# Kernel optimization log

Measured on AMD Instinct MI355X. Metric: run time of the kernel, lower is better.

## Reference

```python
import jax, jax.numpy as jnp
import numpy as np

NUM_TAGS = 32            # init arg
N = NUM_TAGS + 2         # internal num_tags (start/end appended)
START = N - 2
END = N - 1
B = 1024
T = 1024
NEG = -6969.0            # module's 'minus infinity' constant


def setup_inputs() -> dict:
    key = jax.random.key(0)
    k1, k2 = jax.random.split(key)
    features = jax.random.normal(k1, (B, T, N), dtype=jnp.float32)
    # learned parameter: transition matrix [N, N]
    transitions = jax.random.normal(k2, (N, N), dtype=jnp.float32)
    return {"features": features, "transitions": transitions}


def _viterbi(features, transitions):
    # features: [B, T, N]; transitions: [N, N]
    Bn, Tn, Nn = features.shape
    init = jnp.full((Bn, Nn), NEG, dtype=features.dtype).at[:, START].set(0.0)

    def step(scores, feat):
        # score[b, j, k] = scores[b, k] + feat[b, j] + transitions[j, k]
        sc = scores[:, None, :] + feat[:, :, None] + transitions[None, :, :]
        return jnp.max(sc, axis=-1), jnp.argmax(sc, axis=-1)

    feats_t = jnp.swapaxes(features, 0, 1)            # [T, B, N]
    scores, paths = jax.lax.scan(step, init, feats_t)  # paths: [T, B, N] int

    scores = scores + transitions[END]                # add transition to end tag
    best = jnp.max(scores, axis=-1)                   # [B]
    idx = jnp.argmax(scores, axis=-1)                 # [B]

    # backtrack through backpointers, from t = T-1 down to 0
    def back(i, path):
        ni = jnp.take_along_axis(path, i[:, None], axis=1)[:, 0]
        return ni, ni

    _, tags = jax.lax.scan(back, idx, paths, reverse=True)  # tags: [T, B]
    best_path = jnp.concatenate([tags.T, idx[:, None]], axis=1)  # [B, T+1]
    return best, best_path


def reference(features, transitions):
    return _viterbi(features, transitions)
```

## Files before the change

### kernel.cpp

```cpp
#include <hip/hip_runtime.h>
#include <stdint.h>

#define BB 1024
#define TT 1024
#define NN 34
#define NEGV -6969.0f

typedef float v2f __attribute__((ext_vector_type(2)));
typedef float v4f __attribute__((ext_vector_type(4)));

__device__ __forceinline__ float fmax3(float a, float b, float c) {
    return fmaxf(fmaxf(a, b), c);
}

__global__ __launch_bounds__(256, 1) void viterbi_wave(
        const float* __restrict__ feat,
        const float* __restrict__ trans,
        unsigned char* __restrict__ bpg,
        float* __restrict__ out)
{
    __shared__ __align__(16) float sc[4][64];
    __shared__ unsigned char Fm[4][16][NN];
    __shared__ int Eb[4][16];

    const int wid  = threadIdx.x >> 6;
    const int lane = threadIdx.x & 63;
    const int j    = lane;
    const int jm   = (j < NN) ? j : (NN - 1);
    const bool act = (j < NN);
    const int bg   = blockIdx.x * 4 + wid;

    v4f t4[8]; v2f t2;
    {
        const float* trow = trans + jm * NN;
#pragma unroll
        for (int i = 0; i < 8; ++i)
            t4[i] = (v4f){trow[4*i], trow[4*i+1], trow[4*i+2], trow[4*i+3]};
        t2 = (v2f){trow[32], trow[33]};
    }
    v4f e4[8]; v2f e2;
    {
        const float* erow = trans + (NN - 1) * NN;
#pragma unroll
        for (int i = 0; i < 8; ++i)
            e4[i] = (v4f){erow[4*i], erow[4*i+1], erow[4*i+2], erow[4*i+3]};
        e2 = (v2f){erow[32], erow[33]};
    }

    const float* fp = feat + (size_t)bg * TT * NN + jm;
    unsigned char* bpt = bpg + (size_t)bg * TT * NN + j;

    float* const scW = &sc[wid][0];
    const v4f* const S4 = (const v4f*)scW;
    const v2f* const S2 = (const v2f*)scW;

    scW[lane] = (lane == 32) ? 0.0f : NEGV;

    v4f q[8]; v2f q8;
#pragma unroll
    for (int i = 0; i < 8; ++i) q[i] = S4[i];
    q8 = S2[16];

    float fr0 = fp[0*NN], fr1 = fp[1*NN], fr2 = fp[2*NN], fr3 = fp[3*NN];

    auto vstep = [&](float fv, unsigned char* bpw) {
        const v4f f4 = (v4f){fv, fv, fv, fv};
        const v2f f2 = (v2f){fv, fv};
        v4f w[8]; v2f w8;
#pragma unroll
        for (int i = 0; i < 8; ++i) w[i] = (q[i] + f4) + t4[i];
        w8 = (q8 + f2) + t2;
        float wv[NN];
#pragma unroll
        for (int i = 0; i < 8; ++i) {
            wv[4*i+0] = w[i].x; wv[4*i+1] = w[i].y;
            wv[4*i+2] = w[i].z; wv[4*i+3] = w[i].w;
        }
        wv[32] = w8.x; wv[33] = w8.y;
        float a[12];
#pragma unroll
        for (int i = 0; i < 11; ++i) a[i] = fmax3(wv[3*i], wv[3*i+1], wv[3*i+2]);
        a[11] = wv[33];
        float b0 = fmax3(a[0], a[1], a[2]), b1 = fmax3(a[3], a[4], a[5]);
        float b2 = fmax3(a[6], a[7], a[8]), b3 = fmax3(a[9], a[10], a[11]);
        float m = fmaxf(fmaxf(b0, b1), fmaxf(b2, b3));
        scW[lane] = m;
#pragma unroll
        for (int i = 0; i < 8; ++i) q[i] = S4[i];
        q8 = S2[16];
        int am = 127;
#pragma unroll
        for (int k = NN - 1; k >= 0; --k) am = (wv[k] == m) ? k : am;
        if (act) *bpw = (unsigned char)am;
    };

    for (int n = 0; n < 255; ++n) {
        { float f = fr0; fr0 = fp[4*NN]; vstep(f, bpt + 0*NN); }
        { float f = fr1; fr1 = fp[5*NN]; vstep(f, bpt + 1*NN); }
        { float f = fr2; fr2 = fp[6*NN]; vstep(f, bpt + 2*NN); }
        { float f = fr3; fr3 = fp[7*NN]; vstep(f, bpt + 3*NN); }
        fp += 4*NN; bpt += 4*NN;
    }
    vstep(fr0, bpt + 0*NN);
    vstep(fr1, bpt + 1*NN);
    vstep(fr2, bpt + 2*NN);
    vstep(fr3, bpt + 3*NN);

    int bi;
    float bm;
    {
        v4f w[8]; v2f w8;
#pragma unroll
        for (int i = 0; i < 8; ++i) w[i] = q[i] + e4[i];
        w8 = q8 + e2;
        float wv[NN];
#pragma unroll
        for (int i = 0; i < 8; ++i) {
            wv[4*i+0] = w[i].x; wv[4*i+1] = w[i].y;
            wv[4*i+2] = w[i].z; wv[4*i+3] = w[i].w;
        }
        wv[32] = w8.x; wv[33] = w8.y;
        float a[12];
#pragma unroll
        for (int i = 0; i < 11; ++i) a[i] = fmax3(wv[3*i], wv[3*i+1], wv[3*i+2]);
        a[11] = wv[33];
        float b0 = fmax3(a[0], a[1], a[2]), b1 = fmax3(a[3], a[4], a[5]);
        float b2 = fmax3(a[6], a[7], a[8]), b3 = fmax3(a[9], a[10], a[11]);
        bm = fmaxf(fmaxf(b0, b1), fmaxf(b2, b3));
        bi = 127;
#pragma unroll
        for (int k = NN - 1; k >= 0; --k) bi = (wv[k] == bm) ? k : bi;
    }
    if (lane == 0) out[bg] = bm;

    asm volatile("s_waitcnt vmcnt(0)" ::: "memory");
    const unsigned char* __restrict__ bb = bpg + (size_t)bg * TT * NN;

    {
        const int c = lane >> 2;
        const int sub = lane & 3;
        int mv[9];
#pragma unroll
        for (int qi = 0; qi < 9; ++qi) {
            int x = sub + 4 * qi;
            mv[qi] = (x < NN) ? x : (NN - 1);
        }
        const unsigned char* cb = bb + (size_t)c * 64 * NN;
        for (int i = 63; i >= 0; --i) {
            const unsigned char* rb = cb + (size_t)i * NN;
#pragma unroll
            for (int qi = 0; qi < 9; ++qi) mv[qi] = rb[mv[qi]];
        }
#pragma unroll
        for (int qi = 0; qi < 9; ++qi) {
            int x = sub + 4 * qi;
            if (x < NN) Fm[wid][c][x] = (unsigned char)mv[qi];
        }
    }

    if (lane == 0) {
        int e = bi;
        Eb[wid][15] = e;
        for (int c = 15; c >= 1; --c) { e = Fm[wid][c][e]; Eb[wid][c - 1] = e; }
    }

    float* po = out + BB + (size_t)bg * (TT + 1);
    if (lane < 16) {
        int c = lane;
        int m = Eb[wid][c];
        for (int i = 63; i >= 0; --i) {
            m = bb[(size_t)((c * 64 + i) * NN) + m];
            po[c * 64 + i] = (float)m;
        }
    }
    if (lane == 16) po[TT] = (float)bi;
}

extern "C" void kernel_launch(void* const* d_in, const int* in_sizes, int n_in,
                              void* d_out, int out_size, void* d_ws, size_t ws_size,
                              hipStream_t stream) {
    const float* feat  = (const float*)d_in[0];
    const float* trans = (const float*)d_in[1];
    float* out = (float*)d_out;
    unsigned char* bp = (unsigned char*)d_ws;

    viterbi_wave<<<BB / 4, 256, 0, stream>>>(feat, trans, bp, out);
}
```

Baseline: 626.8 us.

## Launch one wave per block and tree-reduce the argmax

Changes the launch from 256-thread blocks holding four independent waves to 64-thread blocks with one wave each, so there are 1024 blocks instead of 256 and waves are scheduled independently. The serial 34-step argmax select chain is replaced by a compare-to-index pass followed by a min3 tree reduction, which shortens the dependency chain on the per-step critical path. A scheduling barrier is added after the shared-memory reload, and the end-transition row is read from global memory at the end rather than held in registers, which lowers register pressure during the main loop. The trade-off is more instructions per step for the argmax and a shift in how waves are placed across CUs.

```diff
diff --git a/kernel.cpp b/kernel.cpp
--- a/kernel.cpp
+++ b/kernel.cpp
@@ -12,23 +12,26 @@
 __device__ __forceinline__ float fmax3(float a, float b, float c) {
     return fmaxf(fmaxf(a, b), c);
 }
+__device__ __forceinline__ int imin2(int a, int b) { return a < b ? a : b; }
+__device__ __forceinline__ int imin3(int a, int b, int c) {
+    return imin2(imin2(a, b), c);
+}
 
-__global__ __launch_bounds__(256, 1) void viterbi_wave(
+__global__ __launch_bounds__(64, 1) void viterbi_wave(
         const float* __restrict__ feat,
         const float* __restrict__ trans,
         unsigned char* __restrict__ bpg,
         float* __restrict__ out)
 {
-    __shared__ __align__(16) float sc[4][64];
-    __shared__ unsigned char Fm[4][16][NN];
-    __shared__ int Eb[4][16];
+    __shared__ __align__(16) float scW[64];
+    __shared__ unsigned char Fm[16][NN];
+    __shared__ int Eb[16];
 
-    const int wid  = threadIdx.x >> 6;
     const int lane = threadIdx.x & 63;
     const int j    = lane;
     const int jm   = (j < NN) ? j : (NN - 1);
     const bool act = (j < NN);
-    const int bg   = blockIdx.x * 4 + wid;
+    const int bg   = blockIdx.x;
 
     v4f t4[8]; v2f t2;
     {
@@ -38,19 +41,10 @@
             t4[i] = (v4f){trow[4*i], trow[4*i+1], trow[4*i+2], trow[4*i+3]};
         t2 = (v2f){trow[32], trow[33]};
     }
-    v4f e4[8]; v2f e2;
-    {
-        const float* erow = trans + (NN - 1) * NN;
-#pragma unroll
-        for (int i = 0; i < 8; ++i)
-            e4[i] = (v4f){erow[4*i], erow[4*i+1], erow[4*i+2], erow[4*i+3]};
-        e2 = (v2f){erow[32], erow[33]};
-    }
 
     const float* fp = feat + (size_t)bg * TT * NN + jm;
     unsigned char* bpt = bpg + (size_t)bg * TT * NN + j;
 
-    float* const scW = &sc[wid][0];
     const v4f* const S4 = (const v4f*)scW;
     const v2f* const S2 = (const v2f*)scW;
 
@@ -88,9 +82,17 @@
 #pragma unroll
         for (int i = 0; i < 8; ++i) q[i] = S4[i];
         q8 = S2[16];
-        int am = 127;
+        __builtin_amdgcn_sched_barrier(0);
+        int e[NN];
 #pragma unroll
-        for (int k = NN - 1; k >= 0; --k) am = (wv[k] == m) ? k : am;
+        for (int k = 0; k < NN; ++k) e[k] = (wv[k] == m) ? k : 127;
+        int r[12];
+#pragma unroll
+        for (int i = 0; i < 11; ++i) r[i] = imin3(e[3*i], e[3*i+1], e[3*i+2]);
+        r[11] = e[33];
+        int s0 = imin3(r[0], r[1], r[2]),  s1 = imin3(r[3], r[4], r[5]);
+        int s2 = imin3(r[6], r[7], r[8]),  s3 = imin3(r[9], r[10], r[11]);
+        int am = imin2(imin2(s0, s1), imin2(s2, s3));
         if (act) *bpw = (unsigned char)am;
     };
 
@@ -109,17 +111,17 @@
     int bi;
     float bm;
     {
-        v4f w[8]; v2f w8;
-#pragma unroll
-        for (int i = 0; i < 8; ++i) w[i] = q[i] + e4[i];
-        w8 = q8 + e2;
+        const float* er = trans + (NN - 1) * NN;
         float wv[NN];
+        float qv[NN];
 #pragma unroll
         for (int i = 0; i < 8; ++i) {
-            wv[4*i+0] = w[i].x; wv[4*i+1] = w[i].y;
-            wv[4*i+2] = w[i].z; wv[4*i+3] = w[i].w;
+            qv[4*i+0] = q[i].x; qv[4*i+1] = q[i].y;
+            qv[4*i+2] = q[i].z; qv[4*i+3] = q[i].w;
         }
-        wv[32] = w8.x; wv[33] = w8.y;
+        qv[32] = q8.x; qv[33] = q8.y;
+#pragma unroll
+        for (int k = 0; k < NN; ++k) wv[k] = qv[k] + er[k];
         float a[12];
 #pragma unroll
         for (int i = 0; i < 11; ++i) a[i] = fmax3(wv[3*i], wv[3*i+1], wv[3*i+2]);
@@ -127,9 +129,16 @@
         float b0 = fmax3(a[0], a[1], a[2]), b1 = fmax3(a[3], a[4], a[5]);
         float b2 = fmax3(a[6], a[7], a[8]), b3 = fmax3(a[9], a[10], a[11]);
         bm = fmaxf(fmaxf(b0, b1), fmaxf(b2, b3));
-        bi = 127;
+        int e[NN];
 #pragma unroll
-        for (int k = NN - 1; k >= 0; --k) bi = (wv[k] == bm) ? k : bi;
+        for (int k = 0; k < NN; ++k) e[k] = (wv[k] == bm) ? k : 127;
+        int r[12];
+#pragma unroll
+        for (int i = 0; i < 11; ++i) r[i] = imin3(e[3*i], e[3*i+1], e[3*i+2]);
+        r[11] = e[33];
+        int s0 = imin3(r[0], r[1], r[2]),  s1 = imin3(r[3], r[4], r[5]);
+        int s2 = imin3(r[6], r[7], r[8]),  s3 = imin3(r[9], r[10], r[11]);
+        bi = imin2(imin2(s0, s1), imin2(s2, s3));
     }
     if (lane == 0) out[bg] = bm;
 
@@ -154,20 +163,20 @@
 #pragma unroll
         for (int qi = 0; qi < 9; ++qi) {
             int x = sub + 4 * qi;
-            if (x < NN) Fm[wid][c][x] = (unsigned char)mv[qi];
+            if (x < NN) Fm[c][x] = (unsigned char)mv[qi];
         }
     }
 
     if (lane == 0) {
         int e = bi;
-        Eb[wid][15] = e;
-        for (int c = 15; c >= 1; --c) { e = Fm[wid][c][e]; Eb[wid][c - 1] = e; }
+        Eb[15] = e;
+        for (int c = 15; c >= 1; --c) { e = Fm[c][e]; Eb[c - 1] = e; }
     }
 
     float* po = out + BB + (size_t)bg * (TT + 1);
     if (lane < 16) {
         int c = lane;
-        int m = Eb[wid][c];
+        int m = Eb[c];
         for (int i = 63; i >= 0; --i) {
             m = bb[(size_t)((c * 64 + i) * NN) + m];
             po[c * 64 + i] = (float)m;
@@ -184,5 +193,5 @@
     float* out = (float*)d_out;
     unsigned char* bp = (unsigned char*)d_ws;
 
-    viterbi_wave<<<BB / 4, 256, 0, stream>>>(feat, trans, bp, out);
+    viterbi_wave<<<BB, 64, 0, stream>>>(feat, trans, bp, out);
 }
```

New measurement: 634.1 us. Within noise of the previous version (+1.2%).
